# Kernel tuning notes

Hardware: AMD Instinct MI355X
Metric: run time of the kernel (lower is better)

## Reference

```python
import jax, jax.numpy as jnp
import numpy as np


def setup_inputs() -> dict:
    key = jax.random.key(0)
    k1, k2, k3 = jax.random.split(key, 3)
    B, T = 4096, 8192
    X = jax.random.normal(k1, (B, T), dtype=jnp.float32)
    raw_a = jax.random.normal(k2, (), dtype=jnp.float32)
    raw_b = jax.random.normal(k3, (), dtype=jnp.float32)
    return {"X": X, "raw_a": raw_a, "raw_b": raw_b}


def reference(X, raw_a, raw_b):
    # project: a = 0.5*tanh(raw_a); per-step input u_t = a * x_t
    # forward step: z_t = u_t + b * z_{t-1},  b = tanh(raw_b),  z_0 = 0
    # readout: squeeze the size-1 hidden dim (already scalar here)
    a = 0.5 * jnp.tanh(raw_a)
    b = jnp.tanh(raw_b)
    u = a * X                      # [B, T]
    mult = jnp.full_like(u, b)     # constant decay per step

    # Affine composition: (m1, s1) then (m2, s2) -> (m2*m1, m2*s1 + s2)
    def combine(c1, c2):
        m1, s1 = c1
        m2, s2 = c2
        return (m1 * m2, m2 * s1 + s2)

    _, Z = jax.lax.associative_scan(combine, (mult, u), axis=1)
    return Z  # [B, T] hidden states over all timesteps
```

## Files before the change

### kernel.cpp

```cpp
#include <hip/hip_runtime.h>
#include <math.h>


typedef float f32x4 __attribute__((ext_vector_type(4)));

#define T_LEN 8192
#define NSUB  8

__global__ __launch_bounds__(256) void lincell_scan(
    const float* __restrict__ X,
    const float* __restrict__ pa,
    const float* __restrict__ pb,
    float* __restrict__ Z,
    int nrows)
{
    __shared__ float wsum[4];

    const int row  = blockIdx.x;
    const int tid  = threadIdx.x;
    const int wave = tid >> 6;
    const int lane = tid & 63;
    if (row >= nrows) return;

    const float a  = 0.5f * tanhf(pa[0]);
    const float b  = tanhf(pb[0]);
    const float b2 = b * b;
    const float b3 = b2 * b;
    const float b4 = b2 * b2;

    const float m1  = b4;
    const float m2  = m1  * m1;
    const float m4  = m2  * m2;
    const float m8  = m4  * m4;
    const float m16 = m8  * m8;
    const float m32 = m16 * m16;
    const float b256  = m32 * m32;
    const float b2048 = b256 * b256 * b256 * b256 * b256 * b256 * b256 * b256;
    const float mstep[6] = { m1, m2, m4, m8, m16, m32 };

    float b4lane = 1.0f;
    b4lane *= (lane & 1)  ? m1  : 1.0f;
    b4lane *= (lane & 2)  ? m2  : 1.0f;
    b4lane *= (lane & 4)  ? m4  : 1.0f;
    b4lane *= (lane & 8)  ? m8  : 1.0f;
    b4lane *= (lane & 16) ? m16 : 1.0f;
    b4lane *= (lane & 32) ? m32 : 1.0f;

    const f32x4* xrow = (const f32x4*)(X + (size_t)row * T_LEN);
    f32x4*       zrow = (f32x4*)(Z + (size_t)row * T_LEN);

    const int vbase = wave * 512 + lane;
    f32x4 v[NSUB];
#pragma unroll
    for (int j = 0; j < NSUB; ++j) v[j] = xrow[vbase + j * 64];

    float y0[NSUB], y1[NSUB], y2[NSUB], y3[NSUB], s[NSUB];
#pragma unroll
    for (int j = 0; j < NSUB; ++j) {
        y0[j] = a * v[j].x;
        y1[j] = fmaf(b, y0[j], a * v[j].y);
        y2[j] = fmaf(b, y1[j], a * v[j].z);
        y3[j] = fmaf(b, y2[j], a * v[j].w);
        s[j]  = y3[j];
    }

#pragma unroll
    for (int k = 0; k < 6; ++k) {
#pragma unroll
        for (int j = 0; j < NSUB; ++j) {
            float t = __shfl_up(s[j], (unsigned)(1 << k), 64);
            t = (lane >= (1 << k)) ? t : 0.0f;
            s[j] = fmaf(mstep[k], t, s[j]);
        }
    }
    float excl[NSUB], tot[NSUB];
#pragma unroll
    for (int j = 0; j < NSUB; ++j) {
        float e = __shfl_up(s[j], 1u, 64);
        excl[j] = (lane >= 1) ? e : 0.0f;
        tot[j]  = __shfl(s[j], 63, 64);
    }

    float Wt = tot[0];
#pragma unroll
    for (int j = 1; j < NSUB; ++j) Wt = fmaf(b256, Wt, tot[j]);
    if (lane == 0) wsum[wave] = Wt;
    __syncthreads();

    float carry = 0.0f;
    if (wave > 0) carry = wsum[0];
    if (wave > 1) carry = fmaf(b2048, carry, wsum[1]);
    if (wave > 2) carry = fmaf(b2048, carry, wsum[2]);

    float cj = carry;
#pragma unroll
    for (int j = 0; j < NSUB; ++j) {
        const float pre = fmaf(b4lane, cj, excl[j]);
        f32x4 o;
        o.x = fmaf(b,  pre, y0[j]);
        o.y = fmaf(b2, pre, y1[j]);
        o.z = fmaf(b3, pre, y2[j]);
        o.w = fmaf(b4, pre, y3[j]);
        __builtin_nontemporal_store(o, &zrow[vbase + j * 64]);
        cj = fmaf(b256, cj, tot[j]);
    }
}

extern "C" void kernel_launch(void* const* d_in, const int* in_sizes, int n_in,
                              void* d_out, int out_size, void* d_ws, size_t ws_size,
                              hipStream_t stream) {
    const float* X  = (const float*)d_in[0];
    const float* pa = (const float*)d_in[1];
    const float* pb = (const float*)d_in[2];
    float* Z = (float*)d_out;

    const int nrows = in_sizes[0] / T_LEN;
    lincell_scan<<<nrows, 256, 0, stream>>>(X, pa, pb, Z, nrows);
}
```

Baseline: 239.2 us.

## Stage row loads through LDS via global_load_lds with 8 waves per block

Loads each row into shared memory with direct global-to-LDS 16-byte loads, then reads the vectors back from LDS. Moves from 4 to 8 waves per block, with 4 sub-chunks per wave, and the cross-wave carry now chains over 8 partial sums. Also replaces the nontemporal stores with plain stores. The aim is more memory parallelism and a less register-heavy load path, at the cost of 32 KB LDS per block, which may limit occupancy.

```diff
diff --git a/kernel.cpp b/kernel.cpp
--- a/kernel.cpp
+++ b/kernel.cpp
@@ -5,22 +5,42 @@
 typedef float f32x4 __attribute__((ext_vector_type(4)));
 
 #define T_LEN 8192
-#define NSUB  8
+#define NSUB  4
+#define WPB   8
+#define WELEM 1024
 
-__global__ __launch_bounds__(256) void lincell_scan(
+__device__ __forceinline__ void gload_lds16(const float* g, float* l) {
+    __builtin_amdgcn_global_load_lds(
+        (const __attribute__((address_space(1))) void*)g,
+        (__attribute__((address_space(3))) void*)l, 16, 0, 0);
+}
+
+__global__ __launch_bounds__(512) void lincell_scan(
     const float* __restrict__ X,
     const float* __restrict__ pa,
     const float* __restrict__ pb,
     float* __restrict__ Z,
     int nrows)
 {
-    __shared__ float wsum[4];
+    __shared__ float lds[T_LEN];
+    __shared__ float wsum[WPB];
 
     const int row  = blockIdx.x;
     const int tid  = threadIdx.x;
     const int wave = tid >> 6;
     const int lane = tid & 63;
     if (row >= nrows) return;
+
+    const float* xrow = X + (size_t)row * T_LEN;
+    float*       zrow = Z + (size_t)row * T_LEN;
+
+    {
+        const float* g = xrow + wave * WELEM + lane * 4;
+        float*       l = lds + wave * WELEM;
+#pragma unroll
+        for (int j = 0; j < NSUB; ++j)
+            gload_lds16(g + j * 256, l + j * 256);
+    }
 
     const float a  = 0.5f * tanhf(pa[0]);
     const float b  = tanhf(pb[0]);
@@ -35,7 +55,7 @@
     const float m16 = m8  * m8;
     const float m32 = m16 * m16;
     const float b256  = m32 * m32;
-    const float b2048 = b256 * b256 * b256 * b256 * b256 * b256 * b256 * b256;
+    const float b1024 = b256 * b256 * b256 * b256;
     const float mstep[6] = { m1, m2, m4, m8, m16, m32 };
 
     float b4lane = 1.0f;
@@ -46,13 +66,13 @@
     b4lane *= (lane & 16) ? m16 : 1.0f;
     b4lane *= (lane & 32) ? m32 : 1.0f;
 
-    const f32x4* xrow = (const f32x4*)(X + (size_t)row * T_LEN);
-    f32x4*       zrow = (f32x4*)(Z + (size_t)row * T_LEN);
+    asm volatile("s_waitcnt vmcnt(0)" ::: "memory");
 
-    const int vbase = wave * 512 + lane;
+    const f32x4* lf4 = (const f32x4*)lds;
     f32x4 v[NSUB];
 #pragma unroll
-    for (int j = 0; j < NSUB; ++j) v[j] = xrow[vbase + j * 64];
+    for (int j = 0; j < NSUB; ++j)
+        v[j] = lf4[wave * 256 + j * 64 + lane];
 
     float y0[NSUB], y1[NSUB], y2[NSUB], y3[NSUB], s[NSUB];
 #pragma unroll
@@ -88,10 +108,11 @@
     __syncthreads();
 
     float carry = 0.0f;
-    if (wave > 0) carry = wsum[0];
-    if (wave > 1) carry = fmaf(b2048, carry, wsum[1]);
-    if (wave > 2) carry = fmaf(b2048, carry, wsum[2]);
+#pragma unroll
+    for (int k = 0; k < WPB - 1; ++k)
+        carry = (wave > k) ? fmaf(b1024, carry, wsum[k]) : carry;
 
+    f32x4* zf4 = (f32x4*)zrow;
     float cj = carry;
 #pragma unroll
     for (int j = 0; j < NSUB; ++j) {
@@ -101,7 +122,7 @@
         o.y = fmaf(b2, pre, y1[j]);
         o.z = fmaf(b3, pre, y2[j]);
         o.w = fmaf(b4, pre, y3[j]);
-        __builtin_nontemporal_store(o, &zrow[vbase + j * 64]);
+        zf4[wave * 256 + j * 64 + lane] = o;
         cj = fmaf(b256, cj, tot[j]);
     }
 }
@@ -115,5 +136,5 @@
     float* Z = (float*)d_out;
 
     const int nrows = in_sizes[0] / T_LEN;
-    lincell_scan<<<nrows, 256, 0, stream>>>(X, pa, pb, Z, nrows);
+    lincell_scan<<<nrows, 512, 0, stream>>>(X, pa, pb, Z, nrows);
 }
```

Result: faster. 233.5 us (-2.4%).
